# Performance work log

Measured on AMD Instinct MI355X. Metric: run time of the kernel, lower is better.

Reference implementation:

```python
import jax, jax.numpy as jnp
import numpy as np

N_NODES = 50000
N_EDGES = 600000
D_IN = 128
D_OUT = 128
P_DROP = 0.1
BN_EPS = 1e-5


def setup_inputs() -> dict:
    key = jax.random.key(0)
    ks = jax.random.split(key, 6)
    x = jax.random.normal(ks[0], (N_NODES, D_IN), dtype=jnp.float32)
    weight = jax.random.normal(ks[1], (D_IN, D_OUT), dtype=jnp.float32) * (1.0 / np.sqrt(D_IN))
    bias = jnp.zeros((D_OUT,), dtype=jnp.float32)
    gamma = jnp.ones((D_OUT,), dtype=jnp.float32)
    beta = jnp.zeros((D_OUT,), dtype=jnp.float32)
    dropout_u = jax.random.uniform(ks[2], (N_NODES, D_OUT), dtype=jnp.float32)
    edge_index = jax.random.randint(ks[3], (2, N_EDGES), 0, N_NODES, dtype=jnp.int64)
    return {"x": x, "weight": weight, "bias": bias, "gamma": gamma,
            "beta": beta, "dropout_u": dropout_u, "edge_index": edge_index}


def reference(x, weight, bias, gamma, beta, dropout_u, edge_index):
    N = x.shape[0]
    # --- GCNConv (add_self_loops=True, symmetric normalization) ---
    loop = jnp.arange(N, dtype=edge_index.dtype)
    src = jnp.concatenate([edge_index[0], loop])  # [E+N]
    dst = jnp.concatenate([edge_index[1], loop])  # [E+N]
    xw = x @ weight                               # [N, D_OUT] small GEMM
    deg = jnp.zeros((N,), dtype=xw.dtype).at[dst].add(1.0)
    dinv = jnp.where(deg > 0, jax.lax.rsqrt(jnp.maximum(deg, 1.0)), 0.0)
    norm = dinv[src] * dinv[dst]                  # [E+N]
    msgs = xw[src] * norm[:, None]                # gather: [E+N, D_OUT]
    z = jax.ops.segment_sum(msgs, dst, num_segments=N) + bias
    # --- activation -> BatchNorm (training stats) -> dropout ---
    z = jax.nn.relu(z)
    mean = jnp.mean(z, axis=0)
    var = jnp.mean((z - mean) ** 2, axis=0)       # biased var, as BN uses
    z = (z - mean) * jax.lax.rsqrt(var + BN_EPS) * gamma + beta
    keep = (dropout_u > P_DROP).astype(z.dtype)
    z = z * keep * (1.0 / (1.0 - P_DROP))
    return z.astype(x.dtype)
```

## Files before the change

### kernel.cpp

```cpp
#include <hip/hip_runtime.h>
#include <cstdint>
#include <cstddef>

#define D 128
#define P_DROP 0.1f
#define INV_KEEP (1.0f / 0.9f)
#define BN_EPS 1e-5f

typedef __attribute__((ext_vector_type(8))) short bf16x8;
typedef __attribute__((ext_vector_type(4))) float f32x4;

__device__ __forceinline__ unsigned f2bf(float f) {
    unsigned u = __float_as_uint(f);
    return (u + 0x7fffu + ((u >> 16) & 1u)) >> 16;
}
__device__ __forceinline__ float bf_lo(unsigned v) { return __uint_as_float(v << 16); }
__device__ __forceinline__ float bf_hi(unsigned v) { return __uint_as_float(v & 0xffff0000u); }

__global__ void k_init(int* __restrict__ hist, int N,
                       float* __restrict__ bnacc,
                       unsigned short* __restrict__ xwb,
                       const float* __restrict__ w,
                       unsigned short* __restrict__ wbf) {
    int stride = gridDim.x * blockDim.x;
    int i0 = blockIdx.x * blockDim.x + threadIdx.x;
    for (int i = i0; i < N; i += stride) hist[i] = 0;
    for (int i = i0; i < 4096; i += stride) bnacc[i] = 0.f;
    for (int i = i0; i < 16384; i += stride) {
        int n = i & 127, k = i >> 7;
        wbf[n * 128 + k] = (unsigned short)f2bf(w[(size_t)k * 128 + n]);
    }
    if (i0 < 64) ((unsigned*)(xwb + (size_t)N * D))[i0] = 0u;
}

__global__ void k_hist(const int* __restrict__ dst, int* __restrict__ hist, int E) {
    int i = blockIdx.x * blockDim.x + threadIdx.x;
    if (i < E) atomicAdd(&hist[dst[i]], 1);
}

__global__ void k_scanA(const int* __restrict__ hist, int* __restrict__ tmp,
                        int* __restrict__ blocksum, int N) {
    __shared__ int sd[256];
    int tid = threadIdx.x;
    int i = blockIdx.x * 256 + tid;
    sd[tid] = (i < N) ? ((hist[i] + 7) & ~7) : 0;
    __syncthreads();
    for (int o = 1; o < 256; o <<= 1) {
        int t = (tid >= o) ? sd[tid - o] : 0;
        __syncthreads();
        sd[tid] += t;
        __syncthreads();
    }
    tmp[i] = sd[tid];
    if (tid == 255) blocksum[blockIdx.x] = sd[255];
}

__global__ void k_scanBC(const int* __restrict__ tmp, const int* __restrict__ blocksum,
                         const int* __restrict__ hist,
                         int* __restrict__ rowptr, int* __restrict__ cursor,
                         unsigned short* __restrict__ ssrc,
                         int N, int NBLK, int sent) {
    __shared__ int sd[256];
    int tid = threadIdx.x;
    int b = blockIdx.x;
    sd[tid] = (tid < NBLK && tid < b) ? blocksum[tid] : 0;
    __syncthreads();
    for (int o = 128; o > 0; o >>= 1) {
        if (tid < o) sd[tid] += sd[tid + o];
        __syncthreads();
    }
    int boff = sd[0];
    int i = b * 256 + tid;
    if (i < N) {
        int deg = hist[i];
        int pd = (deg + 7) & ~7;
        int r = tmp[i] + boff - pd;
        rowptr[i] = r;
        cursor[i] = r;
        for (int k = deg; k < pd; ++k) ssrc[r + k] = (unsigned short)sent;
    }
}

__global__ void k_place(const int* __restrict__ src, const int* __restrict__ dst,
                        int* __restrict__ cursor, unsigned short* __restrict__ ssrc,
                        int E, int N) {
    int g = blockIdx.x & 7;
    int gid = blockIdx.x >> 3;
    int G = gridDim.x >> 3;
    int lo = (int)((long long)N * g >> 3);
    int hi = (int)((long long)N * (g + 1) >> 3);
    for (int i = gid * blockDim.x + threadIdx.x; i < E; i += G * blockDim.x) {
        int d = dst[i];
        if (d >= lo && d < hi) {
            int p = atomicAdd(&cursor[d], 1);
            ssrc[p] = (unsigned short)src[i];
        }
    }
}

__global__ __launch_bounds__(256) void k_gemm(
    const float* __restrict__ x, const unsigned short* __restrict__ wbf,
    const int* __restrict__ hist, unsigned short* __restrict__ xwb,
    float* __restrict__ dinv, int N) {
    __shared__ unsigned short xs[64][136];
    __shared__ unsigned short wt[128][136];
    int tid = threadIdx.x;
    int row0 = blockIdx.x * 64;

#pragma unroll
    for (int i = 0; i < 8; ++i) {
        int flat = tid + i * 256;
        int n = flat >> 4;
        int ko = (flat & 15) * 8;
        *(uint4*)&wt[n][ko] = *(const uint4*)&wbf[n * 128 + ko];
    }
#pragma unroll
    for (int i = 0; i < 8; ++i) {
        int flat = tid + i * 256;
        int r = flat >> 5;
        int kq = flat & 31;
        int row = row0 + r;
        float4 v = (row < N) ? *(const float4*)&x[(size_t)row * D + kq * 4]
                             : make_float4(0.f, 0.f, 0.f, 0.f);
        uint2 pk;
        pk.x = f2bf(v.x) | (f2bf(v.y) << 16);
        pk.y = f2bf(v.z) | (f2bf(v.w) << 16);
        *(uint2*)&xs[r][kq * 4] = pk;
    }
    __syncthreads();

    int wv = tid >> 6, lane = tid & 63;
    int l15 = lane & 15, quad = lane >> 4;
    int mrow = wv * 16 + l15;
    f32x4 acc[8];
#pragma unroll
    for (int t = 0; t < 8; ++t) acc[t] = (f32x4){0.f, 0.f, 0.f, 0.f};
#pragma unroll
    for (int k0 = 0; k0 < D; k0 += 32) {
        bf16x8 af = *(bf16x8*)&xs[mrow][k0 + quad * 8];
#pragma unroll
        for (int nt = 0; nt < 8; ++nt) {
            bf16x8 bfr = *(bf16x8*)&wt[nt * 16 + l15][k0 + quad * 8];
            acc[nt] = __builtin_amdgcn_mfma_f32_16x16x32_bf16(af, bfr, acc[nt], 0, 0, 0);
        }
    }
#pragma unroll
    for (int reg = 0; reg < 4; ++reg) {
        int node = row0 + wv * 16 + quad * 4 + reg;
        if (node < N) {
            float dv = rsqrtf((float)(hist[node] + 1));
            if (l15 == 0) dinv[node] = dv;
#pragma unroll
            for (int nt = 0; nt < 8; ++nt) {
                float val = acc[nt][reg] * dv;
                xwb[(size_t)node * D + nt * 16 + l15] = (unsigned short)f2bf(val);
            }
        }
    }
}

__global__ __launch_bounds__(256) void k_aggregate(
    const unsigned short* __restrict__ xwb, const float* __restrict__ dinv,
    const unsigned short* __restrict__ ssrc, const int* __restrict__ rowptr,
    const int* __restrict__ hist, const float* __restrict__ bias,
    float* __restrict__ y, float* __restrict__ bnacc, int N) {
    int tid = threadIdx.x;
    int lane = tid & 63;
    int wv = tid >> 6;
    int w0 = blockIdx.x * 4 + wv;
    int totw = gridDim.x * 4;
    float2 b2 = *(const float2*)(bias + lane * 2);
    float s0 = 0.f, s1 = 0.f, q0 = 0.f, q1 = 0.f;

    int n = w0;
    int baseC = 0, degC = 0, vsC = 0;
    if (n < N) {
        baseC = rowptr[n];
        degC = hist[n];
        vsC = (int)ssrc[baseC + lane];
    }
    int np = n + totw;
    int baseP = 0, degP = 0;
    if (np < N) { baseP = rowptr[np]; degP = hist[np]; }

    while (n < N) {
        int nn = __builtin_amdgcn_readfirstlane(n);
        int vsP = 0;
        if (np < N) vsP = (int)ssrc[baseP + lane];
        int n2 = np + totw;
        int base2 = 0, deg2 = 0;
        if (n2 < N) { base2 = rowptr[n2]; deg2 = hist[n2]; }
        unsigned sv = *(const unsigned*)(xwb + (size_t)nn * D + lane * 2);
        int pdeg = (degC + 7) & ~7;
        float a0 = 0.f, a1 = 0.f;
        int lim0 = min(64, pdeg);
        for (int j0 = 0; j0 < lim0; j0 += 8) {
            unsigned vr[8];
#pragma unroll
            for (int j = 0; j < 8; ++j) {
                int idx = __builtin_amdgcn_readlane(vsC, j0 + j);
                vr[j] = *(const unsigned*)(xwb + (size_t)idx * D + lane * 2);
            }
#pragma unroll
            for (int j = 0; j < 8; ++j) { a0 += bf_lo(vr[j]); a1 += bf_hi(vr[j]); }
        }
        for (int c0 = 64; c0 < pdeg; c0 += 64) {
            int vs2 = (int)ssrc[baseC + c0 + lane];
            int lim = min(64, pdeg - c0);
            for (int j0 = 0; j0 < lim; j0 += 8) {
                unsigned vr[8];
#pragma unroll
                for (int j = 0; j < 8; ++j) {
                    int idx = __builtin_amdgcn_readlane(vs2, j0 + j);
                    vr[j] = *(const unsigned*)(xwb + (size_t)idx * D + lane * 2);
                }
#pragma unroll
                for (int j = 0; j < 8; ++j) { a0 += bf_lo(vr[j]); a1 += bf_hi(vr[j]); }
            }
        }
        a0 += bf_lo(sv); a1 += bf_hi(sv);
        float dv = dinv[nn];
        float z0 = fmaxf(fmaf(a0, dv, b2.x), 0.f);
        float z1 = fmaxf(fmaf(a1, dv, b2.y), 0.f);
        *(float2*)(y + (size_t)nn * D + lane * 2) = make_float2(z0, z1);
        s0 += z0; s1 += z1; q0 += z0 * z0; q1 += z1 * z1;
        n = np; baseC = baseP; degC = degP; vsC = vsP;
        np = n2; baseP = base2; degP = deg2;
    }

    __shared__ float red[256][4];
    red[tid][0] = s0; red[tid][1] = s1; red[tid][2] = q0; red[tid][3] = q1;
    __syncthreads();
    int o = tid;
    int col = o & 127;
    int l = col >> 1;
    int si = ((o >= 128) ? 2 : 0) + (col & 1);
    float acc = red[0 * 64 + l][si] + red[1 * 64 + l][si] +
                red[2 * 64 + l][si] + red[3 * 64 + l][si];
    atomicAdd(bnacc + 256 * (blockIdx.x & 15) + o, acc);
}

__global__ __launch_bounds__(256) void k_finalize(
    float* __restrict__ out, const float* __restrict__ u,
    const float* __restrict__ bnacc, const float* __restrict__ gamma,
    const float* __restrict__ beta, int total4, float invN) {
    __shared__ float sc[128], sh[128];
    int tid = threadIdx.x;
    if (tid < 128) {
        float sm = 0.f, sq = 0.f;
#pragma unroll
        for (int k = 0; k < 16; ++k) {
            sm += bnacc[k * 256 + tid];
            sq += bnacc[k * 256 + 128 + tid];
        }
        float mean = sm * invN;
        float var = fmaxf(sq * invN - mean * mean, 0.f);
        float s = gamma[tid] * rsqrtf(var + BN_EPS);
        sc[tid] = s;
        sh[tid] = beta[tid] - mean * s;
    }
    __syncthreads();
    int stride = gridDim.x * 256;
    for (int i = blockIdx.x * 256 + tid; i < total4; i += stride) {
        float4 v = ((const float4*)out)[i];
        float4 uu = ((const float4*)u)[i];
        int c = (i & 31) * 4;
        v.x = fmaf(v.x, sc[c],     sh[c])     * (uu.x > P_DROP ? INV_KEEP : 0.f);
        v.y = fmaf(v.y, sc[c + 1], sh[c + 1]) * (uu.y > P_DROP ? INV_KEEP : 0.f);
        v.z = fmaf(v.z, sc[c + 2], sh[c + 2]) * (uu.z > P_DROP ? INV_KEEP : 0.f);
        v.w = fmaf(v.w, sc[c + 3], sh[c + 3]) * (uu.w > P_DROP ? INV_KEEP : 0.f);
        ((float4*)out)[i] = v;
    }
}

extern "C" void kernel_launch(void* const* d_in, const int* in_sizes, int n_in,
                              void* d_out, int out_size, void* d_ws, size_t ws_size,
                              hipStream_t stream) {
    const float* x      = (const float*)d_in[0];
    const float* weight = (const float*)d_in[1];
    const float* bias   = (const float*)d_in[2];
    const float* gamma  = (const float*)d_in[3];
    const float* beta   = (const float*)d_in[4];
    const float* du     = (const float*)d_in[5];
    const int*   eidx   = (const int*)d_in[6];
    float* out = (float*)d_out;

    const int N = in_sizes[0] / D;
    const int E = in_sizes[6] / 2;
    const int* esrc = eidx;
    const int* edst = eidx + E;

    char* p = (char*)d_ws;
    auto alloc = [&](size_t bytes) {
        char* q = p;
        p += (bytes + 255) & ~(size_t)255;
        return q;
    };
    unsigned short* xwb = (unsigned short*)alloc((size_t)(N + 1) * D * sizeof(unsigned short));
    int*   hist     = (int*)alloc((size_t)N * sizeof(int));
    int*   cursor   = (int*)alloc((size_t)N * sizeof(int));
    int*   rowptr   = (int*)alloc((size_t)N * sizeof(int));
    const int NBLK = (N + 255) / 256;
    int*   tmp      = (int*)alloc((size_t)NBLK * 256 * sizeof(int));
    int*   blocksum = (int*)alloc((size_t)NBLK * sizeof(int));
    const int PS = E + 7 * N + 128;
    unsigned short* ssrc = (unsigned short*)alloc((size_t)PS * sizeof(unsigned short));
    float* dinv     = (float*)alloc((size_t)N * sizeof(float));
    float* bnacc    = (float*)alloc(16 * 256 * sizeof(float));
    unsigned short* wbf = (unsigned short*)alloc(16384 * sizeof(unsigned short));

    const int EB = (E + 255) / 256;
    const int total4 = N * (D / 4);

    hipLaunchKernelGGL(k_init, dim3(256), dim3(256), 0, stream,
                       hist, N, bnacc, xwb, weight, wbf);
    hipLaunchKernelGGL(k_hist, dim3(EB), dim3(256), 0, stream, edst, hist, E);
    hipLaunchKernelGGL(k_scanA, dim3(NBLK), dim3(256), 0, stream, hist, tmp, blocksum, N);
    hipLaunchKernelGGL(k_scanBC, dim3(NBLK), dim3(256), 0, stream,
                       tmp, blocksum, hist, rowptr, cursor, ssrc, N, NBLK, N);
    hipLaunchKernelGGL(k_place, dim3(1024), dim3(256), 0, stream, esrc, edst, cursor, ssrc, E, N);
    hipLaunchKernelGGL(k_gemm, dim3((N + 63) / 64), dim3(256), 0, stream,
                       x, wbf, hist, xwb, dinv, N);
    hipLaunchKernelGGL(k_aggregate, dim3(2048), dim3(256), 0, stream,
                       xwb, dinv, ssrc, rowptr, hist, bias, out, bnacc, N);
    hipLaunchKernelGGL(k_finalize, dim3(2048), dim3(256), 0, stream,
                       out, du, bnacc, gamma, beta, total4, 1.0f / (float)N);
}
```

Before: 208.7 us.

## Merge scan into one kernel and co-schedule edge placement with GEMM

The two-pass block scan is replaced by a single kernel in which each block recomputes its prefix offset by summing all earlier histogram entries, then scans 4096 entries locally. The edge-placement pass and the bf16 GEMM now run in one launch, with the first 1024 blocks doing placement and the rest doing GEMM tiles. Together this removes two kernel launches and lets the atomic-bound placement work overlap with the MFMA GEMM. In exchange, later scan blocks redundantly reread a growing prefix of the histogram, and the fused kernel carries the GEMM's shared-memory allocation for the placement blocks too, which can lower their occupancy.

```diff
diff --git a/kernel.cpp b/kernel.cpp
--- a/kernel.cpp
+++ b/kernel.cpp
@@ -6,6 +6,7 @@
 #define P_DROP 0.1f
 #define INV_KEEP (1.0f / 0.9f)
 #define BN_EPS 1e-5f
+#define PBLK 1024
 
 typedef __attribute__((ext_vector_type(8))) short bf16x8;
 typedef __attribute__((ext_vector_type(4))) float f32x4;
@@ -38,75 +39,79 @@
     if (i < E) atomicAdd(&hist[dst[i]], 1);
 }
 
-__global__ void k_scanA(const int* __restrict__ hist, int* __restrict__ tmp,
-                        int* __restrict__ blocksum, int N) {
-    __shared__ int sd[256];
+__global__ __launch_bounds__(256) void k_scan(
+    const int* __restrict__ hist, int* __restrict__ rowptr, int* __restrict__ cursor,
+    unsigned short* __restrict__ ssrc, int N, int sent) {
+    __shared__ int rs[256];
     int tid = threadIdx.x;
-    int i = blockIdx.x * 256 + tid;
-    sd[tid] = (i < N) ? ((hist[i] + 7) & ~7) : 0;
+    int pre = blockIdx.x * 4096;
+    int acc = 0;
+    for (int i = tid; i < pre; i += 256) acc += (hist[i] + 7) & ~7;
+    rs[tid] = acc;
+    __syncthreads();
+    for (int o = 128; o > 0; o >>= 1) {
+        if (tid < o) rs[tid] += rs[tid + o];
+        __syncthreads();
+    }
+    int boff = rs[0];
+    __syncthreads();
+    int base = pre + tid * 16;
+    int tsum = 0;
+#pragma unroll
+    for (int j = 0; j < 16; ++j) {
+        int i = base + j;
+        if (i < N) tsum += (hist[i] + 7) & ~7;
+    }
+    rs[tid] = tsum;
     __syncthreads();
     for (int o = 1; o < 256; o <<= 1) {
-        int t = (tid >= o) ? sd[tid - o] : 0;
+        int t = (tid >= o) ? rs[tid - o] : 0;
         __syncthreads();
-        sd[tid] += t;
+        rs[tid] += t;
         __syncthreads();
     }
-    tmp[i] = sd[tid];
-    if (tid == 255) blocksum[blockIdx.x] = sd[255];
-}
-
-__global__ void k_scanBC(const int* __restrict__ tmp, const int* __restrict__ blocksum,
-                         const int* __restrict__ hist,
-                         int* __restrict__ rowptr, int* __restrict__ cursor,
-                         unsigned short* __restrict__ ssrc,
-                         int N, int NBLK, int sent) {
-    __shared__ int sd[256];
-    int tid = threadIdx.x;
-    int b = blockIdx.x;
-    sd[tid] = (tid < NBLK && tid < b) ? blocksum[tid] : 0;
-    __syncthreads();
-    for (int o = 128; o > 0; o >>= 1) {
-        if (tid < o) sd[tid] += sd[tid + o];
-        __syncthreads();
-    }
-    int boff = sd[0];
-    int i = b * 256 + tid;
-    if (i < N) {
-        int deg = hist[i];
-        int pd = (deg + 7) & ~7;
-        int r = tmp[i] + boff - pd;
-        rowptr[i] = r;
-        cursor[i] = r;
-        for (int k = deg; k < pd; ++k) ssrc[r + k] = (unsigned short)sent;
-    }
-}
-
-__global__ void k_place(const int* __restrict__ src, const int* __restrict__ dst,
-                        int* __restrict__ cursor, unsigned short* __restrict__ ssrc,
-                        int E, int N) {
-    int g = blockIdx.x & 7;
-    int gid = blockIdx.x >> 3;
-    int G = gridDim.x >> 3;
-    int lo = (int)((long long)N * g >> 3);
-    int hi = (int)((long long)N * (g + 1) >> 3);
-    for (int i = gid * blockDim.x + threadIdx.x; i < E; i += G * blockDim.x) {
-        int d = dst[i];
-        if (d >= lo && d < hi) {
-            int p = atomicAdd(&cursor[d], 1);
-            ssrc[p] = (unsigned short)src[i];
-        }
-    }
-}
-
-__global__ __launch_bounds__(256) void k_gemm(
+    int run = boff + rs[tid] - tsum;
+#pragma unroll
+    for (int j = 0; j < 16; ++j) {
+        int i = base + j;
+        if (i < N) {
+            int deg = hist[i];
+            int pd = (deg + 7) & ~7;
+            rowptr[i] = run;
+            cursor[i] = run;
+            for (int k = deg; k < pd; ++k) ssrc[run + k] = (unsigned short)sent;
+            run += pd;
+        }
+    }
+}
+
+__global__ __launch_bounds__(256) void k_place_gemm(
+    const int* __restrict__ src, const int* __restrict__ dst,
+    int* __restrict__ cursor, unsigned short* __restrict__ ssrc, int E,
     const float* __restrict__ x, const unsigned short* __restrict__ wbf,
     const int* __restrict__ hist, unsigned short* __restrict__ xwb,
     float* __restrict__ dinv, int N) {
     __shared__ unsigned short xs[64][136];
     __shared__ unsigned short wt[128][136];
     int tid = threadIdx.x;
-    int row0 = blockIdx.x * 64;
-
+
+    if (blockIdx.x < PBLK) {
+        int g = blockIdx.x & 7;
+        int gid = blockIdx.x >> 3;
+        const int G = PBLK >> 3;
+        int lo = (int)((long long)N * g >> 3);
+        int hi = (int)((long long)N * (g + 1) >> 3);
+        for (int i = gid * 256 + tid; i < E; i += G * 256) {
+            int d = dst[i];
+            if (d >= lo && d < hi) {
+                int p = atomicAdd(&cursor[d], 1);
+                ssrc[p] = (unsigned short)src[i];
+            }
+        }
+        return;
+    }
+
+    int row0 = (blockIdx.x - PBLK) * 64;
 #pragma unroll
     for (int i = 0; i < 8; ++i) {
         int flat = tid + i * 256;
@@ -300,9 +305,6 @@
     int*   hist     = (int*)alloc((size_t)N * sizeof(int));
     int*   cursor   = (int*)alloc((size_t)N * sizeof(int));
     int*   rowptr   = (int*)alloc((size_t)N * sizeof(int));
-    const int NBLK = (N + 255) / 256;
-    int*   tmp      = (int*)alloc((size_t)NBLK * 256 * sizeof(int));
-    int*   blocksum = (int*)alloc((size_t)NBLK * sizeof(int));
     const int PS = E + 7 * N + 128;
     unsigned short* ssrc = (unsigned short*)alloc((size_t)PS * sizeof(unsigned short));
     float* dinv     = (float*)alloc((size_t)N * sizeof(float));
@@ -311,15 +313,16 @@
 
     const int EB = (E + 255) / 256;
     const int total4 = N * (D / 4);
+    const int NB2 = (N + 4095) / 4096;
+    const int GB = (N + 63) / 64;
 
     hipLaunchKernelGGL(k_init, dim3(256), dim3(256), 0, stream,
                        hist, N, bnacc, xwb, weight, wbf);
     hipLaunchKernelGGL(k_hist, dim3(EB), dim3(256), 0, stream, edst, hist, E);
-    hipLaunchKernelGGL(k_scanA, dim3(NBLK), dim3(256), 0, stream, hist, tmp, blocksum, N);
-    hipLaunchKernelGGL(k_scanBC, dim3(NBLK), dim3(256), 0, stream,
-                       tmp, blocksum, hist, rowptr, cursor, ssrc, N, NBLK, N);
-    hipLaunchKernelGGL(k_place, dim3(1024), dim3(256), 0, stream, esrc, edst, cursor, ssrc, E, N);
-    hipLaunchKernelGGL(k_gemm, dim3((N + 63) / 64), dim3(256), 0, stream,
+    hipLaunchKernelGGL(k_scan, dim3(NB2), dim3(256), 0, stream,
+                       hist, rowptr, cursor, ssrc, N, N);
+    hipLaunchKernelGGL(k_place_gemm, dim3(PBLK + GB), dim3(256), 0, stream,
+                       esrc, edst, cursor, ssrc, E,
                        x, wbf, hist, xwb, dinv, N);
     hipLaunchKernelGGL(k_aggregate, dim3(2048), dim3(256), 0, stream,
                        xwb, dinv, ssrc, rowptr, hist, bias, out, bnacc, N);
```

After: 243.5 us. 16.7% more time.

## Merge edge placement and GEMM into one launch; read weights from global

Applied to the files above, without the earlier changes.

The edge-placement scatter and the bf16 MFMA GEMM become one kernel. The first 1024 blocks do placement and the remaining blocks compute xw rows, which removes a launch boundary and lets the two independent phases run at the same time. The GEMM no longer stages the weight matrix in LDS and reads B fragments straight from global memory, which cuts LDS use and raises occupancy. In exchange, weight reads may hit L2 more often and the fused kernel's occupancy is set by the GEMM's shared-memory footprint.

```diff
diff --git a/kernel.cpp b/kernel.cpp
--- a/kernel.cpp
+++ b/kernel.cpp
@@ -6,6 +6,7 @@
 #define P_DROP 0.1f
 #define INV_KEEP (1.0f / 0.9f)
 #define BN_EPS 1e-5f
+#define PBLK 1024
 
 typedef __attribute__((ext_vector_type(8))) short bf16x8;
 typedef __attribute__((ext_vector_type(4))) float f32x4;
@@ -81,39 +82,32 @@
     }
 }
 
-__global__ void k_place(const int* __restrict__ src, const int* __restrict__ dst,
-                        int* __restrict__ cursor, unsigned short* __restrict__ ssrc,
-                        int E, int N) {
-    int g = blockIdx.x & 7;
-    int gid = blockIdx.x >> 3;
-    int G = gridDim.x >> 3;
-    int lo = (int)((long long)N * g >> 3);
-    int hi = (int)((long long)N * (g + 1) >> 3);
-    for (int i = gid * blockDim.x + threadIdx.x; i < E; i += G * blockDim.x) {
-        int d = dst[i];
-        if (d >= lo && d < hi) {
-            int p = atomicAdd(&cursor[d], 1);
-            ssrc[p] = (unsigned short)src[i];
-        }
-    }
-}
-
-__global__ __launch_bounds__(256) void k_gemm(
+__global__ __launch_bounds__(256) void k_place_gemm(
+    const int* __restrict__ src, const int* __restrict__ dst,
+    int* __restrict__ cursor, unsigned short* __restrict__ ssrc, int E,
     const float* __restrict__ x, const unsigned short* __restrict__ wbf,
     const int* __restrict__ hist, unsigned short* __restrict__ xwb,
     float* __restrict__ dinv, int N) {
     __shared__ unsigned short xs[64][136];
-    __shared__ unsigned short wt[128][136];
-    int tid = threadIdx.x;
-    int row0 = blockIdx.x * 64;
-
-#pragma unroll
-    for (int i = 0; i < 8; ++i) {
-        int flat = tid + i * 256;
-        int n = flat >> 4;
-        int ko = (flat & 15) * 8;
-        *(uint4*)&wt[n][ko] = *(const uint4*)&wbf[n * 128 + ko];
-    }
+    int tid = threadIdx.x;
+
+    if (blockIdx.x < PBLK) {
+        int g = blockIdx.x & 7;
+        int gid = blockIdx.x >> 3;
+        const int G = PBLK >> 3;
+        int lo = (int)((long long)N * g >> 3);
+        int hi = (int)((long long)N * (g + 1) >> 3);
+        for (int i = gid * 256 + tid; i < E; i += G * 256) {
+            int d = dst[i];
+            if (d >= lo && d < hi) {
+                int p = atomicAdd(&cursor[d], 1);
+                ssrc[p] = (unsigned short)src[i];
+            }
+        }
+        return;
+    }
+
+    int row0 = (blockIdx.x - PBLK) * 64;
 #pragma unroll
     for (int i = 0; i < 8; ++i) {
         int flat = tid + i * 256;
@@ -132,6 +126,7 @@
     int wv = tid >> 6, lane = tid & 63;
     int l15 = lane & 15, quad = lane >> 4;
     int mrow = wv * 16 + l15;
+    const unsigned short* wrow = wbf + (size_t)l15 * 128 + quad * 8;
     f32x4 acc[8];
 #pragma unroll
     for (int t = 0; t < 8; ++t) acc[t] = (f32x4){0.f, 0.f, 0.f, 0.f};
@@ -140,7 +135,7 @@
         bf16x8 af = *(bf16x8*)&xs[mrow][k0 + quad * 8];
 #pragma unroll
         for (int nt = 0; nt < 8; ++nt) {
-            bf16x8 bfr = *(bf16x8*)&wt[nt * 16 + l15][k0 + quad * 8];
+            bf16x8 bfr = *(const bf16x8*)(wrow + (size_t)nt * 16 * 128 + k0);
             acc[nt] = __builtin_amdgcn_mfma_f32_16x16x32_bf16(af, bfr, acc[nt], 0, 0, 0);
         }
     }
@@ -311,6 +306,7 @@
 
     const int EB = (E + 255) / 256;
     const int total4 = N * (D / 4);
+    const int GB = (N + 63) / 64;
 
     hipLaunchKernelGGL(k_init, dim3(256), dim3(256), 0, stream,
                        hist, N, bnacc, xwb, weight, wbf);
@@ -318,8 +314,8 @@
     hipLaunchKernelGGL(k_scanA, dim3(NBLK), dim3(256), 0, stream, hist, tmp, blocksum, N);
     hipLaunchKernelGGL(k_scanBC, dim3(NBLK), dim3(256), 0, stream,
                        tmp, blocksum, hist, rowptr, cursor, ssrc, N, NBLK, N);
-    hipLaunchKernelGGL(k_place, dim3(1024), dim3(256), 0, stream, esrc, edst, cursor, ssrc, E, N);
-    hipLaunchKernelGGL(k_gemm, dim3((N + 63) / 64), dim3(256), 0, stream,
+    hipLaunchKernelGGL(k_place_gemm, dim3(PBLK + GB), dim3(256), 0, stream,
+                       esrc, edst, cursor, ssrc, E,
                        x, wbf, hist, xwb, dinv, N);
     hipLaunchKernelGGL(k_aggregate, dim3(2048), dim3(256), 0, stream,
                        xwb, dinv, ssrc, rowptr, hist, bias, out, bnacc, N);
```

Result: slower. 216.9 us (+3.9%).
